# Performance work log

Measured on AMD Instinct MI355X. Metric: run time of the kernel, lower is better.

The kernel has to match this reference:

```python
import jax, jax.numpy as jnp
import numpy as np

# Skeleton bones flattened across the 4 groups of VarLoss
_ID1 = np.array([3, 2, 4, 5, 16, 15, 11, 12, 1, 4, 14, 11])
_ID2 = np.array([2, 1, 5, 6, 15, 14, 12, 13, 0, 0, 8, 8])
_W = np.array([1.0085885098415446, 1.0, 1.0, 1.0085885098415446,
               1.1375361376887123, 1.0, 1.0, 1.1375361376887123,
               1.0, 1.0, 1.0, 1.0], dtype=np.float32)
_GID = np.array([0, 0, 0, 0, 1, 1, 1, 1, 2, 2, 3, 3])
_ONEHOT = np.eye(4, dtype=np.float32)[_GID]  # [12 bones, 4 groups]
_VAR_WEIGHT = 1.0


def setup_inputs() -> dict:
    key = jax.random.key(0)
    k1, k2, k3, k4 = jax.random.split(key, 4)
    B, J, H, W = 8192, 17, 64, 64
    output = jax.random.normal(k1, (B, 1, H, W), dtype=jnp.float32)
    mask = jnp.zeros((B, J), dtype=jnp.float32)  # sum==0 -> loss active
    ind = jax.random.randint(k2, (B, J), 0, H * W, dtype=jnp.int64)
    target = jax.random.uniform(k3, (B, J), dtype=jnp.float32)  # visibility in [0,1]
    gt_2d = jax.random.normal(k4, (B, J, 2), dtype=jnp.float32)
    return {"output": output, "mask": mask, "ind": ind, "target": target, "gt_2d": gt_2d}


def reference(output, mask, ind, target, gt_2d):
    B = output.shape[0]
    # _tranpose_and_gather_scalar: C==1 so permute is a no-op on values
    flat = output.reshape(B, -1)                      # [B, H*W]
    pred = jnp.take_along_axis(flat, ind, axis=1)     # [B, J]

    xy = gt_2d.reshape(B, -1, 2)                      # [B, J, 2]
    id1, id2 = jnp.asarray(_ID1), jnp.asarray(_ID2)
    w = jnp.asarray(_W)
    onehot = jnp.asarray(_ONEHOT)                     # [12, 4]

    vis = (target[:, id1] > 0.5) & (target[:, id2] > 0.5)      # [B, 12]
    d2 = jnp.sum((xy[:, id1] - xy[:, id2]) ** 2, axis=-1) \
         + (pred[:, id1] - pred[:, id2]) ** 2                   # [B, 12]
    l = jnp.where(vis, jnp.sqrt(jnp.where(vis, d2, 1.0)) * w, 0.0)

    num = vis.astype(jnp.float32) @ onehot            # [B, 4] bones visible per group
    sum_l = l @ onehot                                # [B, 4]
    E = sum_l / jnp.maximum(num, 1.0)                 # mean bone length per group
    E_b = E @ onehot.T                                # broadcast back to bones [B,12]
    num_b = num @ onehot.T                            # [B, 12]

    contrib = jnp.where(vis & (l > 0),
                        (l - E_b) ** 2 / (2.0 * jnp.maximum(num_b, 1.0)),
                        0.0)
    per_sample = contrib.sum(axis=-1)                 # [B]

    active = (mask.sum(axis=1) == 0)                  # [B]
    loss = _VAR_WEIGHT * jnp.where(active, per_sample, 0.0).sum() / B
    return loss.reshape((1,))
```

## Files before the change

kernel.cpp:

```cpp
#include <hip/hip_runtime.h>


#define BLK 64

__global__ __launch_bounds__(BLK) void bone_partial(
    const float* __restrict__ out_hm,
    const float* __restrict__ mask,
    const int*   __restrict__ ind,
    const float* __restrict__ target,
    const float* __restrict__ gt2d,
    float* __restrict__ partial, int B)
{
    constexpr int id1[12]  = {3, 2, 4, 5, 16, 15, 11, 12, 1, 4, 14, 11};
    constexpr int id2[12]  = {2, 1, 5, 6, 15, 14, 12, 13, 0, 0,  8,  8};
    constexpr int gid[12]  = {0, 0, 0, 0,  1,  1,  1,  1, 2, 2,  3,  3};
    const float wbone[12]  = {1.0085885098415446f, 1.0f, 1.0f, 1.0085885098415446f,
                              1.1375361376887123f, 1.0f, 1.0f, 1.1375361376887123f,
                              1.0f, 1.0f, 1.0f, 1.0f};

    const int b = blockIdx.x * BLK + threadIdx.x;
    float per = 0.0f;
    if (b < B) {
        const float*  tb = target + (size_t)b * 17;
        const float*  mb = mask   + (size_t)b * 17;
        const int*    ib = ind    + (size_t)b * 17;
        const float2* gb = (const float2*)(gt2d + (size_t)b * 34);
        const float*  ob = out_hm + (size_t)b * 4096;

        int   idx[17];
        #pragma unroll
        for (int j = 0; j < 17; ++j) idx[j] = ib[j];
        float pr[17];
        #pragma unroll
        for (int j = 0; j < 17; ++j) pr[j] = ob[idx[j]];

        float t[17], gx[17], gy[17];
        #pragma unroll
        for (int j = 0; j < 17; ++j) t[j] = tb[j];
        #pragma unroll
        for (int j = 0; j < 17; ++j) { float2 g = gb[j]; gx[j] = g.x; gy[j] = g.y; }
        float msum = 0.0f;
        #pragma unroll
        for (int j = 0; j < 17; ++j) msum += mb[j];

        float num[4] = {0,0,0,0}, sl[4] = {0,0,0,0};
        float l[12];
        bool  vis[12];
        #pragma unroll
        for (int k = 0; k < 12; ++k) {
            const int a = id1[k], c = id2[k];
            const bool v = (t[a] > 0.5f) && (t[c] > 0.5f);
            const float dx = gx[a] - gx[c];
            const float dy = gy[a] - gy[c];
            const float dp = pr[a] - pr[c];
            const float d2 = dx*dx + dy*dy + dp*dp;
            const float lv = v ? sqrtf(d2) * wbone[k] : 0.0f;
            vis[k] = v; l[k] = lv;
            num[gid[k]] += v ? 1.0f : 0.0f;
            sl[gid[k]]  += lv;
        }
        float E[4], dn[4];
        #pragma unroll
        for (int g = 0; g < 4; ++g) { dn[g] = fmaxf(num[g], 1.0f); E[g] = sl[g] / dn[g]; }
        #pragma unroll
        for (int k = 0; k < 12; ++k) {
            if (vis[k] && l[k] > 0.0f) {
                const float d = l[k] - E[gid[k]];
                per += d * d / (2.0f * dn[gid[k]]);
            }
        }
        if (msum != 0.0f) per = 0.0f;
    }

    #pragma unroll
    for (int off = 32; off > 0; off >>= 1) per += __shfl_down(per, off, 64);
    if (threadIdx.x == 0) partial[blockIdx.x] = per;
}

__global__ __launch_bounds__(64) void bone_finalize(
    const float* __restrict__ partial, int n,
    float* __restrict__ out, float invB)
{
    float s = 0.0f;
    for (int i = threadIdx.x; i < n; i += 64) s += partial[i];
    #pragma unroll
    for (int off = 32; off > 0; off >>= 1) s += __shfl_down(s, off, 64);
    if (threadIdx.x == 0) out[0] = s * invB;
}

extern "C" void kernel_launch(void* const* d_in, const int* in_sizes, int n_in,
                              void* d_out, int out_size, void* d_ws, size_t ws_size,
                              hipStream_t stream)
{
    const float* output = (const float*)d_in[0];
    const float* mask   = (const float*)d_in[1];
    const int*   ind    = (const int*)  d_in[2];
    const float* target = (const float*)d_in[3];
    const float* gt2d   = (const float*)d_in[4];

    const int B    = in_sizes[1] / 17;
    const int nblk = (B + BLK - 1) / BLK;

    float* partial = (float*)d_ws;

    bone_partial<<<nblk, BLK, 0, stream>>>(output, mask, ind, target, gt2d, partial, B);
    bone_finalize<<<1, 64, 0, stream>>>(partial, nblk, (float*)d_out, 1.0f / (float)B);
}
```

Measured before the change: 10.95 us.

## Split each sample's bone loss across two threads by joint subset

Each sample is now handled by a pair of adjacent threads. One thread computes bone groups 0 and 2 over joints 0-6, and the other computes groups 1 and 3 over joints 8 and 11-16. Each thread loads only 7 joints instead of 17, and the two partial mask sums are combined with a lane shuffle. The grid doubles in size to expose more parallelism and shorten each thread's serial gather chain, at the cost of branch divergence within the wave and index remapping through select operations.

```diff
diff --git a/kernel.cpp b/kernel.cpp
--- a/kernel.cpp
+++ b/kernel.cpp
@@ -11,66 +11,93 @@
     const float* __restrict__ gt2d,
     float* __restrict__ partial, int B)
 {
-    constexpr int id1[12]  = {3, 2, 4, 5, 16, 15, 11, 12, 1, 4, 14, 11};
-    constexpr int id2[12]  = {2, 1, 5, 6, 15, 14, 12, 13, 0, 0,  8,  8};
-    constexpr int gid[12]  = {0, 0, 0, 0,  1,  1,  1,  1, 2, 2,  3,  3};
-    const float wbone[12]  = {1.0085885098415446f, 1.0f, 1.0f, 1.0085885098415446f,
-                              1.1375361376887123f, 1.0f, 1.0f, 1.1375361376887123f,
-                              1.0f, 1.0f, 1.0f, 1.0f};
+    const int tid = blockIdx.x * BLK + threadIdx.x;
+    const int p   = tid >> 1;
+    const int h   = tid & 1;
+    float per  = 0.0f;
+    float msum = 0.0f;
 
-    const int b = blockIdx.x * BLK + threadIdx.x;
-    float per = 0.0f;
-    if (b < B) {
-        const float*  tb = target + (size_t)b * 17;
-        const float*  mb = mask   + (size_t)b * 17;
-        const int*    ib = ind    + (size_t)b * 17;
-        const float2* gb = (const float2*)(gt2d + (size_t)b * 34);
-        const float*  ob = out_hm + (size_t)b * 4096;
+    if (p < B) {
+        const float* tb = target + (size_t)p * 17;
+        const float* mb = mask   + (size_t)p * 17;
+        const int*   ib = ind    + (size_t)p * 17;
+        const float* gb = gt2d   + (size_t)p * 34;
+        const float* ob = out_hm + (size_t)p * 4096;
 
-        int   idx[17];
+        int jm[7];
+        jm[0] = h ? 8  : 0;
+        jm[1] = h ? 11 : 1;
+        jm[2] = h ? 12 : 2;
+        jm[3] = h ? 13 : 3;
+        jm[4] = h ? 14 : 4;
+        jm[5] = h ? 15 : 5;
+        jm[6] = h ? 16 : 6;
+
+        int idx[7];
         #pragma unroll
-        for (int j = 0; j < 17; ++j) idx[j] = ib[j];
-        float pr[17];
+        for (int k = 0; k < 7; ++k) idx[k] = ib[jm[k]];
+        float pr[7];
         #pragma unroll
-        for (int j = 0; j < 17; ++j) pr[j] = ob[idx[j]];
+        for (int k = 0; k < 7; ++k) pr[k] = ob[idx[k]];
 
-        float t[17], gx[17], gy[17];
+        float t[7], gx[7], gy[7];
         #pragma unroll
-        for (int j = 0; j < 17; ++j) t[j] = tb[j];
+        for (int k = 0; k < 7; ++k) t[k] = tb[jm[k]];
         #pragma unroll
-        for (int j = 0; j < 17; ++j) { float2 g = gb[j]; gx[j] = g.x; gy[j] = g.y; }
-        float msum = 0.0f;
-        #pragma unroll
-        for (int j = 0; j < 17; ++j) msum += mb[j];
+        for (int k = 0; k < 7; ++k) {
+            float2 g = *(const float2*)(gb + 2 * jm[k]);
+            gx[k] = g.x; gy[k] = g.y;
+        }
 
-        float num[4] = {0,0,0,0}, sl[4] = {0,0,0,0};
-        float l[12];
-        bool  vis[12];
-        #pragma unroll
-        for (int k = 0; k < 12; ++k) {
-            const int a = id1[k], c = id2[k];
-            const bool v = (t[a] > 0.5f) && (t[c] > 0.5f);
+        float numA = 0.f, slA = 0.f, numB = 0.f, slB = 0.f;
+        float l[6]; bool vs[6];
+
+        auto bone = [&](int k, int a, int c, float w, bool grpA) {
+            const bool v  = (t[a] > 0.5f) && (t[c] > 0.5f);
             const float dx = gx[a] - gx[c];
             const float dy = gy[a] - gy[c];
             const float dp = pr[a] - pr[c];
-            const float d2 = dx*dx + dy*dy + dp*dp;
-            const float lv = v ? sqrtf(d2) * wbone[k] : 0.0f;
-            vis[k] = v; l[k] = lv;
-            num[gid[k]] += v ? 1.0f : 0.0f;
-            sl[gid[k]]  += lv;
+            const float lv = v ? sqrtf(dx*dx + dy*dy + dp*dp) * w : 0.f;
+            vs[k] = v; l[k] = lv;
+            if (grpA) { numA += v ? 1.f : 0.f; slA += lv; }
+            else      { numB += v ? 1.f : 0.f; slB += lv; }
+        };
+
+        if (h == 0) {
+            const float W = 1.0085885098415446f;
+            bone(0, 3, 2, W,   true);
+            bone(1, 2, 1, 1.f, true);
+            bone(2, 4, 5, 1.f, true);
+            bone(3, 5, 6, W,   true);
+            bone(4, 1, 0, 1.f, false);
+            bone(5, 4, 0, 1.f, false);
+            msum = mb[0]+mb[1]+mb[2]+mb[3]+mb[4]+mb[5]+mb[6]+mb[7]+mb[8];
+        } else {
+            const float W = 1.1375361376887123f;
+            bone(0, 6, 5, W,   true);
+            bone(1, 5, 4, 1.f, true);
+            bone(2, 1, 2, 1.f, true);
+            bone(3, 2, 3, W,   true);
+            bone(4, 4, 0, 1.f, false);
+            bone(5, 1, 0, 1.f, false);
+            msum = mb[9]+mb[10]+mb[11]+mb[12]+mb[13]+mb[14]+mb[15]+mb[16];
         }
-        float E[4], dn[4];
+
+        const float dnA = fmaxf(numA, 1.f), EA = slA / dnA;
+        const float dnB = fmaxf(numB, 1.f), EB = slB / dnB;
         #pragma unroll
-        for (int g = 0; g < 4; ++g) { dn[g] = fmaxf(num[g], 1.0f); E[g] = sl[g] / dn[g]; }
-        #pragma unroll
-        for (int k = 0; k < 12; ++k) {
-            if (vis[k] && l[k] > 0.0f) {
-                const float d = l[k] - E[gid[k]];
-                per += d * d / (2.0f * dn[gid[k]]);
+        for (int k = 0; k < 6; ++k) {
+            const float E  = (k < 4) ? EA : EB;
+            const float dn = (k < 4) ? dnA : dnB;
+            if (vs[k] && l[k] > 0.f) {
+                const float d = l[k] - E;
+                per += d * d / (2.f * dn);
             }
         }
-        if (msum != 0.0f) per = 0.0f;
     }
+
+    const float mo = __shfl_xor(msum, 1, 64);
+    if (msum + mo != 0.0f) per = 0.0f;
 
     #pragma unroll
     for (int off = 32; off > 0; off >>= 1) per += __shfl_down(per, off, 64);
@@ -99,7 +126,7 @@
     const float* gt2d   = (const float*)d_in[4];
 
     const int B    = in_sizes[1] / 17;
-    const int nblk = (B + BLK - 1) / BLK;
+    const int nblk = (2 * B + BLK - 1) / BLK;
 
     float* partial = (float*)d_ws;
 
```

Result: slower. 11.25 us (+2.7%).
